# Optimization experiments

Hardware: AMD Instinct MI355X
Metric: run time of the kernel (lower is better)

Reference implementation:

```python
import jax, jax.numpy as jnp
import numpy as np

NEG_BIG = -9.0e15  # matches -9000000000000000.0 fill in the torch code


def setup_inputs() -> dict:
    key = jax.random.key(0)
    ks = jax.random.split(key, 8)
    N, Fin, Fout = 8192, 256, 128
    input = jax.random.normal(ks[0], (N, Fin), dtype=jnp.float32)
    adj = jax.random.randint(ks[1], (N, N), 0, 2, dtype=jnp.int32)
    s_fc = 1.0 / np.sqrt(Fin)
    s_at = 1.0 / np.sqrt(Fout)
    W_fc = jax.random.normal(ks[2], (Fin, Fout), dtype=jnp.float32) * s_fc
    b_fc = jax.random.normal(ks[3], (Fout,), dtype=jnp.float32) * s_fc
    w_ax = jax.random.normal(ks[4], (Fout, 1), dtype=jnp.float32) * s_at
    b_ax = jax.random.normal(ks[5], (1,), dtype=jnp.float32) * s_at
    w_an = jax.random.normal(ks[6], (Fout, 1), dtype=jnp.float32) * s_at
    b_an = jax.random.normal(ks[7], (1,), dtype=jnp.float32) * s_at
    return {"input": input, "adj": adj, "W_fc": W_fc, "b_fc": b_fc,
            "w_ax": w_ax, "b_ax": b_ax, "w_an": w_an, "b_an": b_an}


def reference(input, adj, W_fc, b_fc, w_ax, b_ax, w_an, b_an):
    # x = fc(input): [N, Fout]
    x = input @ W_fc + b_fc
    # rank-1 additive scores: att_x(x) [N,1] + att_nei(x).T [1,N] -> [N,N]
    x_att = x @ w_ax + b_ax          # [N, 1]
    neib_att = (x @ w_an + b_an).T   # [1, N]
    ws = x_att + neib_att            # [N, N]
    # adjacency mask + row softmax
    ws = jnp.where(adj > 0, ws, NEG_BIG)
    ws = jax.nn.softmax(ws, axis=1)
    # dense aggregation + residual + ELU (dropout is identity in eval)
    out = jax.nn.elu(x + ws @ x)
    return out
```

## Files before the change

kernel.cpp:

```cpp
#include <hip/hip_runtime.h>
#include <hip/hip_bf16.h>
#include <math.h>


using f32x4  = __attribute__((ext_vector_type(4))) float;
using bf16x8 = __attribute__((ext_vector_type(8))) short;

#define N_NODES 8192
#define FIN     256
#define FOUT    128
#define NPAD    144
#define NSPLIT  8
#define KCHUNK  (N_NODES / NSPLIT)

#define X_OFF    0u
#define T_OFF    (X_OFF + N_NODES*FOUT*4u)
#define PMAX_OFF (T_OFF + N_NODES*4u)
#define GMAX_OFF (PMAX_OFF + 1024u)
#define YT_OFF   (GMAX_OFF + 512u)
#define P_OFF    (YT_OFF + (size_t)NPAD*N_NODES*2u)

__device__ __forceinline__ unsigned short f2bf(float f) {
  unsigned int u = __float_as_uint(f);
  unsigned int r = (u + 0x7FFFu + ((u >> 16) & 1u)) >> 16;
  return (unsigned short)r;
}

__global__ __launch_bounds__(256) void k1_fc(const float* __restrict__ in,
    const float* __restrict__ Wfc, const float* __restrict__ bfc,
    float* __restrict__ x) {
  __shared__ float sm[16 * FIN];
  const int tid = threadIdx.x;
  const int r0  = blockIdx.x * 16;
  const float4* gin = reinterpret_cast<const float4*>(in + (size_t)r0 * FIN);
  float4* sm4 = reinterpret_cast<float4*>(sm);
  #pragma unroll
  for (int i = 0; i < 4; i++) sm4[i * 256 + tid] = gin[i * 256 + tid];
  __syncthreads();
  const int d = tid & 127, g = tid >> 7;
  const float bias = bfc[d];
  float acc[8];
  #pragma unroll
  for (int r = 0; r < 8; r++) acc[r] = bias;
  const float4* s4 = reinterpret_cast<const float4*>(sm);
  for (int k = 0; k < FIN; k += 4) {
    float w0 = Wfc[(k + 0) * FOUT + d];
    float w1 = Wfc[(k + 1) * FOUT + d];
    float w2 = Wfc[(k + 2) * FOUT + d];
    float w3 = Wfc[(k + 3) * FOUT + d];
    #pragma unroll
    for (int r = 0; r < 8; r++) {
      float4 iv = s4[((g * 8 + r) * FIN + k) >> 2];
      acc[r] = fmaf(iv.x, w0, acc[r]);
      acc[r] = fmaf(iv.y, w1, acc[r]);
      acc[r] = fmaf(iv.z, w2, acc[r]);
      acc[r] = fmaf(iv.w, w3, acc[r]);
    }
  }
  #pragma unroll
  for (int r = 0; r < 8; r++)
    x[(size_t)(r0 + g * 8 + r) * FOUT + d] = acc[r];
}

__global__ __launch_bounds__(256) void k2_att(const float* __restrict__ x,
    const float* __restrict__ wan, const float* __restrict__ ban,
    float* __restrict__ t, float* __restrict__ pmax) {
  __shared__ float wm[4];
  const int tid = threadIdx.x, lane = tid & 63, w = tid >> 6;
  const float w0 = wan[lane], w1 = wan[lane + 64];
  const float bb = ban[0];
  float tmax = -1e30f;
  const int rbase = blockIdx.x * 32 + w * 8;
  for (int rr = 0; rr < 8; rr++) {
    const int row = rbase + rr;
    float p = x[(size_t)row * FOUT + lane] * w0
            + x[(size_t)row * FOUT + 64 + lane] * w1;
    #pragma unroll
    for (int m = 1; m < 64; m <<= 1) p += __shfl_xor(p, m);
    const float tv = p + bb;
    if (lane == 0) t[row] = tv;
    tmax = fmaxf(tmax, tv);
  }
  if (lane == 0) wm[w] = tmax;
  __syncthreads();
  if (tid == 0)
    pmax[blockIdx.x] = fmaxf(fmaxf(wm[0], wm[1]), fmaxf(wm[2], wm[3]));
}

__global__ void k3_gmax(const float* __restrict__ pmax, float* __restrict__ gmax) {
  float v = fmaxf(fmaxf(pmax[threadIdx.x], pmax[threadIdx.x + 64]),
                  fmaxf(pmax[threadIdx.x + 128], pmax[threadIdx.x + 192]));
  #pragma unroll
  for (int m = 1; m < 64; m <<= 1) v = fmaxf(v, __shfl_xor(v, m));
  if (threadIdx.x == 0) gmax[0] = v;
}

__global__ __launch_bounds__(256) void k4_y(const float* __restrict__ x,
    const float* __restrict__ t, const float* __restrict__ gmax,
    unsigned short* __restrict__ Yf) {
  __shared__ unsigned short sm[NPAD * 64];
  const int tid = threadIdx.x, lane = tid & 63, w = tid >> 6;
  const int jj = lane, j = blockIdx.x * 64 + jj;
  const float e = expf(t[j] - gmax[0]);
  const float4* x4 = reinterpret_cast<const float4*>(x + (size_t)j * FOUT + w * 32);
  #pragma unroll
  for (int dd = 0; dd < 8; dd++) {
    float4 xv = x4[dd];
    const int c = w * 32 + dd * 4;
    sm[(c + 0) * 64 + jj] = f2bf(e * xv.x);
    sm[(c + 1) * 64 + jj] = f2bf(e * xv.y);
    sm[(c + 2) * 64 + jj] = f2bf(e * xv.z);
    sm[(c + 3) * 64 + jj] = f2bf(e * xv.w);
  }
  #pragma unroll
  for (int i = 0; i < 4; i++) {
    const int c = 128 + w * 4 + i;
    sm[c * 64 + jj] = (c == 128) ? f2bf(e) : (unsigned short)0;
  }
  __syncthreads();
  for (int c5 = w; c5 < 18; c5 += 4) {
    const int wnd = c5 / 9, nf = c5 % 9;
    const int srcIdx = (nf * 16 + (lane & 15)) * 64 + wnd * 32 + (lane >> 4) * 8;
    bf16x8 v = *reinterpret_cast<const bf16x8*>(&sm[srcIdx]);
    const size_t Wg = (size_t)blockIdx.x * 2 + wnd;
    *reinterpret_cast<bf16x8*>(Yf + (Wg * 9 + nf) * 512 + lane * 8) = v;
  }
}

__global__ __launch_bounds__(256) void k5_gemm(const int* __restrict__ adj,
    const unsigned short* __restrict__ Yf, float* __restrict__ P) {
  const int tid  = threadIdx.x;
  const int lane = tid & 63, w = tid >> 6;
  const int bm = blockIdx.x, s = blockIdx.y;
  const int q  = lane >> 4;
  const int arow = bm * 64 + w * 16 + (lane & 15);
  const int* aptr = adj + (size_t)arow * N_NODES + s * KCHUNK + q * 8;
  const unsigned short* bptr = Yf + ((size_t)s * (KCHUNK / 32) * 9) * 512 + lane * 8;

  f32x4 acc[9];
  #pragma unroll
  for (int nf = 0; nf < 9; nf++) acc[nf] = (f32x4){0.f, 0.f, 0.f, 0.f};

#define LOAD_A(dst0, dst1, kk_) \
    dst0 = *reinterpret_cast<const int4*>(aptr + (kk_)); \
    dst1 = *reinterpret_cast<const int4*>(aptr + (kk_) + 4);

#define CONV_MFMA(a0_, a1_, kk_) { \
    bf16x8 bf[9]; \
    const unsigned short* bw = bptr + (size_t)((kk_) >> 5) * 9 * 512; \
    _Pragma("unroll") \
    for (int nf = 0; nf < 9; nf++) \
      bf[nf] = *reinterpret_cast<const bf16x8*>(bw + nf * 512); \
    union { bf16x8 v; unsigned int u[4]; } af; \
    af.u[0] = (unsigned int)((a0_).x | ((a0_).y << 16)) * 0x3F80u; \
    af.u[1] = (unsigned int)((a0_).z | ((a0_).w << 16)) * 0x3F80u; \
    af.u[2] = (unsigned int)((a1_).x | ((a1_).y << 16)) * 0x3F80u; \
    af.u[3] = (unsigned int)((a1_).z | ((a1_).w << 16)) * 0x3F80u; \
    _Pragma("unroll") \
    for (int nf = 0; nf < 9; nf++) \
      acc[nf] = __builtin_amdgcn_mfma_f32_16x16x32_bf16(af.v, bf[nf], acc[nf], 0, 0, 0); \
  }

  int4 A0a, A0b, A1a, A1b, A2a, A2b, A3a, A3b;
  LOAD_A(A0a, A0b, 0);
  LOAD_A(A1a, A1b, 32);
  for (int kk = 0; kk <= KCHUNK - 128; kk += 64) {
    LOAD_A(A2a, A2b, kk + 64);
    CONV_MFMA(A0a, A0b, kk);
    LOAD_A(A3a, A3b, kk + 96);
    CONV_MFMA(A1a, A1b, kk + 32);
    A0a = A2a; A0b = A2b; A1a = A3a; A1b = A3b;
  }
  CONV_MFMA(A0a, A0b, KCHUNK - 64);
  CONV_MFMA(A1a, A1b, KCHUNK - 32);
#undef LOAD_A
#undef CONV_MFMA

  float* Pp = P + (size_t)s * N_NODES * NPAD;
  const int colb = lane & 15;
  #pragma unroll
  for (int nf = 0; nf < 9; nf++) {
    if (nf == 8 && colb != 0) continue;
    #pragma unroll
    for (int r = 0; r < 4; r++) {
      const int grow = bm * 64 + w * 16 + q * 4 + r;
      Pp[(size_t)grow * NPAD + nf * 16 + colb] = acc[nf][r];
    }
  }
}

__global__ __launch_bounds__(256) void k6_fin(const float* __restrict__ P,
    const float* __restrict__ x, float* __restrict__ out) {
  const int gid = blockIdx.x * 256 + threadIdx.x;
  const int i = gid >> 7, d = gid & 127;
  const size_t base = (size_t)i * NPAD;
  float num = 0.f, Z = 0.f;
  #pragma unroll
  for (int s = 0; s < NSPLIT; s++) {
    num += P[(size_t)s * N_NODES * NPAD + base + d];
    Z   += P[(size_t)s * N_NODES * NPAD + base + 128];
  }
  const float agg = (Z > 0.f) ? num / Z : 0.f;
  const float v = x[(size_t)i * FOUT + d] + agg;
  out[gid] = (v > 0.f) ? v : expm1f(v);
}

extern "C" void kernel_launch(void* const* d_in, const int* in_sizes, int n_in,
                              void* d_out, int out_size, void* d_ws, size_t ws_size,
                              hipStream_t stream) {
  const float* input = (const float*)d_in[0];
  const int*   adj   = (const int*)d_in[1];
  const float* Wfc   = (const float*)d_in[2];
  const float* bfc   = (const float*)d_in[3];
  const float* wan   = (const float*)d_in[6];
  const float* ban   = (const float*)d_in[7];

  char* ws = (char*)d_ws;
  float*          x    = (float*)(ws + X_OFF);
  float*          t    = (float*)(ws + T_OFF);
  float*          pmax = (float*)(ws + PMAX_OFF);
  float*          gmax = (float*)(ws + GMAX_OFF);
  unsigned short* Yf   = (unsigned short*)(ws + YT_OFF);
  float*          P    = (float*)(ws + P_OFF);
  float*          out  = (float*)d_out;

  k1_fc  <<<dim3(512),         dim3(256), 0, stream>>>(input, Wfc, bfc, x);
  k2_att <<<dim3(256),         dim3(256), 0, stream>>>(x, wan, ban, t, pmax);
  k3_gmax<<<dim3(1),           dim3(64),  0, stream>>>(pmax, gmax);
  k4_y   <<<dim3(128),         dim3(256), 0, stream>>>(x, t, gmax, Yf);
  k5_gemm<<<dim3(128, NSPLIT), dim3(256), 0, stream>>>(adj, Yf, P);
  k6_fin <<<dim3(4096),        dim3(256), 0, stream>>>(P, x, out);
}
```

Baseline: 482.0 us.

## Stage adjacency tiles into LDS via async global_load_lds with double buffering

The GEMM kernel now loads adjacency tiles into a swizzled, double-buffered LDS area using direct global-to-LDS loads, instead of loading them straight into registers with strided per-lane int4 reads. Fragments are then read from LDS with an XOR swizzle to avoid bank conflicts, and the B fragments are prefetched one step ahead into alternating register sets. The aim is fully coalesced row reads of the large int32 adjacency matrix and overlap of memory with MFMA work. In exchange it adds 32KB of LDS per block and a barrier per iteration, which may reduce occupancy.

```diff
diff --git a/kernel.cpp b/kernel.cpp
--- a/kernel.cpp
+++ b/kernel.cpp
@@ -24,6 +24,12 @@
   unsigned int u = __float_as_uint(f);
   unsigned int r = (u + 0x7FFFu + ((u >> 16) & 1u)) >> 16;
   return (unsigned short)r;
+}
+
+__device__ __forceinline__ void gload_lds16(const void* gsrc, void* ldst) {
+  __builtin_amdgcn_global_load_lds(
+      (const __attribute__((address_space(1))) void*)gsrc,
+      (__attribute__((address_space(3))) void*)ldst, 16, 0, 0);
 }
 
 __global__ __launch_bounds__(256) void k1_fc(const float* __restrict__ in,
@@ -129,28 +135,45 @@
 
 __global__ __launch_bounds__(256) void k5_gemm(const int* __restrict__ adj,
     const unsigned short* __restrict__ Yf, float* __restrict__ P) {
+  __shared__ int ldsA[2][64 * 64];
   const int tid  = threadIdx.x;
   const int lane = tid & 63, w = tid >> 6;
   const int bm = blockIdx.x, s = blockIdx.y;
   const int q  = lane >> 4;
-  const int arow = bm * 64 + w * 16 + (lane & 15);
-  const int* aptr = adj + (size_t)arow * N_NODES + s * KCHUNK + q * 8;
-  const unsigned short* bptr = Yf + ((size_t)s * (KCHUNK / 32) * 9) * 512 + lane * 8;
+  const int rsub = lane >> 4, cb16 = (lane & 15) << 4;
+  const unsigned short* bbase = Yf + (size_t)s * 32 * 9 * 512 + lane * 8;
 
   f32x4 acc[9];
   #pragma unroll
   for (int nf = 0; nf < 9; nf++) acc[nf] = (f32x4){0.f, 0.f, 0.f, 0.f};
 
-#define LOAD_A(dst0, dst1, kk_) \
-    dst0 = *reinterpret_cast<const int4*>(aptr + (kk_)); \
-    dst1 = *reinterpret_cast<const int4*>(aptr + (kk_) + 4);
-
-#define CONV_MFMA(a0_, a1_, kk_) { \
-    bf16x8 bf[9]; \
-    const unsigned short* bw = bptr + (size_t)((kk_) >> 5) * 9 * 512; \
+#define STAGE_A(kbase_, buf_) { \
+    _Pragma("unroll") \
+    for (int i = 0; i < 4; i++) { \
+      const int rit = w * 16 + i * 4 + rsub; \
+      const int gcb = cb16 ^ ((rit & 7) << 4); \
+      const char* gsrc = (const char*)adj + (((size_t)(bm * 64 + rit)) << 15) \
+                       + (size_t)(s * KCHUNK + (kbase_)) * 4 + gcb; \
+      gload_lds16(gsrc, (char*)&ldsA[buf_][(w * 16 + i * 4) * 64]); \
+    } }
+
+#define LOAD_B(dst_, wnd_) { \
+    const unsigned short* p_ = bbase + (size_t)(wnd_) * 9 * 512; \
     _Pragma("unroll") \
     for (int nf = 0; nf < 9; nf++) \
-      bf[nf] = *reinterpret_cast<const bf16x8*>(bw + nf * 512); \
+      dst_[nf] = *reinterpret_cast<const bf16x8*>(p_ + nf * 512); \
+  }
+
+#define AFRAG(buf_, kk_, a0_, a1_) { \
+    const int r_ = lane & 15; \
+    const int sw_ = (r_ & 7) << 4; \
+    const char* rowb_ = (const char*)&ldsA[buf_][(w * 16 + r_) * 64]; \
+    const int cb0_ = ((kk_) + q * 8) * 4; \
+    a0_ = *reinterpret_cast<const int4*>(rowb_ + (cb0_ ^ sw_)); \
+    a1_ = *reinterpret_cast<const int4*>(rowb_ + ((cb0_ + 16) ^ sw_)); \
+  }
+
+#define MFMA9(a0_, a1_, B_) { \
     union { bf16x8 v; unsigned int u[4]; } af; \
     af.u[0] = (unsigned int)((a0_).x | ((a0_).y << 16)) * 0x3F80u; \
     af.u[1] = (unsigned int)((a0_).z | ((a0_).w << 16)) * 0x3F80u; \
@@ -158,23 +181,32 @@
     af.u[3] = (unsigned int)((a1_).z | ((a1_).w << 16)) * 0x3F80u; \
     _Pragma("unroll") \
     for (int nf = 0; nf < 9; nf++) \
-      acc[nf] = __builtin_amdgcn_mfma_f32_16x16x32_bf16(af.v, bf[nf], acc[nf], 0, 0, 0); \
-  }
-
-  int4 A0a, A0b, A1a, A1b, A2a, A2b, A3a, A3b;
-  LOAD_A(A0a, A0b, 0);
-  LOAD_A(A1a, A1b, 32);
-  for (int kk = 0; kk <= KCHUNK - 128; kk += 64) {
-    LOAD_A(A2a, A2b, kk + 64);
-    CONV_MFMA(A0a, A0b, kk);
-    LOAD_A(A3a, A3b, kk + 96);
-    CONV_MFMA(A1a, A1b, kk + 32);
-    A0a = A2a; A0b = A2b; A1a = A3a; A1b = A3b;
-  }
-  CONV_MFMA(A0a, A0b, KCHUNK - 64);
-  CONV_MFMA(A1a, A1b, KCHUNK - 32);
-#undef LOAD_A
-#undef CONV_MFMA
+      acc[nf] = __builtin_amdgcn_mfma_f32_16x16x32_bf16(af.v, B_[nf], acc[nf], 0, 0, 0); \
+  }
+
+  bf16x8 Be[9], Bo[9];
+  int4 a0, a1;
+
+  STAGE_A(0, 0);
+  LOAD_B(Be, 0);
+  LOAD_B(Bo, 1);
+  __syncthreads();
+
+  for (int t = 0; t < 16; ++t) {
+    const int buf = t & 1;
+    if (t < 15) STAGE_A((t + 1) * 64, buf ^ 1);
+    AFRAG(buf, 0, a0, a1);
+    MFMA9(a0, a1, Be);
+    if (t < 15) LOAD_B(Be, 2 * t + 2);
+    AFRAG(buf, 32, a0, a1);
+    MFMA9(a0, a1, Bo);
+    if (t < 15) LOAD_B(Bo, 2 * t + 3);
+    __syncthreads();
+  }
+#undef STAGE_A
+#undef LOAD_B
+#undef AFRAG
+#undef MFMA9
 
   float* Pp = P + (size_t)s * N_NODES * NPAD;
   const int colb = lane & 15;
```

Result: faster. 459.4 us (-4.7%).
